# Kernel optimization log

Hardware: AMD Instinct MI355X
Metric: run time of the kernel (lower is better)

## Reference

```python
import jax, jax.numpy as jnp
import numpy as np

H = 8          # num_heads
D = 64         # head_dim
IN = 512       # input_dim
SCALE = D ** -0.5


def setup_inputs() -> dict:
    key = jax.random.key(0)
    ks = jax.random.split(key, 5)
    b, n = 4, 2048
    inner = H * D
    x = jax.random.normal(ks[0], (b, n, IN), dtype=jnp.float32)
    # nn.Linear weights stored as [out, in]; apply as x @ W.T
    Wq = jax.random.normal(ks[1], (inner, IN), dtype=jnp.float32) * (IN ** -0.5)
    Wkv = jax.random.normal(ks[2], (2 * inner, IN), dtype=jnp.float32) * (IN ** -0.5)
    Wo = jax.random.normal(ks[3], (IN, inner), dtype=jnp.float32) * (inner ** -0.5)
    bo = jax.random.normal(ks[4], (IN,), dtype=jnp.float32) * 0.01
    return {"x": x, "Wq": Wq, "Wkv": Wkv, "Wo": Wo, "bo": bo}


def reference(x, Wq, Wkv, Wo, bo):
    b, n, _ = x.shape
    q = jnp.einsum('bni,oi->bno', x, Wq).reshape(b, n, H, D).transpose(0, 2, 1, 3)
    kv = jnp.einsum('bni,oi->bno', x, Wkv)
    k, v = jnp.split(kv, 2, axis=-1)
    k = k.reshape(b, n, H, D).transpose(0, 2, 1, 3)
    v = v.reshape(b, n, H, D).transpose(0, 2, 1, 3)
    attn = jax.nn.softmax(jnp.einsum('bhnd,bhmd->bhnm', q, k) * SCALE, axis=-1)
    # dropout in eval mode: identity
    out = jnp.einsum('bhnm,bhmd->bhnd', attn, v)
    out = out.transpose(0, 2, 1, 3).reshape(b, n, H * D)
    return jnp.einsum('bno,io->bni', out, Wo) + bo
```

## Files before the change

### kernel.cpp

```cpp
#include <hip/hip_runtime.h>
#include <hip/hip_bf16.h>

#define H_ 8
#define D_ 64
#define IN_ 512
#define B_ 4
#define N_ 2048
#define TOK_ (B_*N_)
#define CLOG2_ 0.18033688011112042f

typedef __attribute__((ext_vector_type(8))) short short8;
typedef __attribute__((ext_vector_type(4))) short bs4;
typedef __attribute__((ext_vector_type(4))) float f32x4;

__device__ __forceinline__ unsigned short f2bf(float f) {
  unsigned int u = __float_as_uint(f);
  u += 0x7FFFu + ((u >> 16) & 1u);
  return (unsigned short)(u >> 16);
}

__device__ __forceinline__ short8 cvt8(const float4 a, const float4 b) {
  union { short8 v; __hip_bfloat162 h[4]; } z;
  z.h[0] = __float22bfloat162_rn(make_float2(a.x, a.y));
  z.h[1] = __float22bfloat162_rn(make_float2(a.z, a.w));
  z.h[2] = __float22bfloat162_rn(make_float2(b.x, b.y));
  z.h[3] = __float22bfloat162_rn(make_float2(b.z, b.w));
  return z.v;
}

__device__ __forceinline__ bs4 pack4(float a, float b, float c, float d) {
  union { bs4 v; __hip_bfloat162 h[2]; } z;
  z.h[0] = __float22bfloat162_rn(make_float2(a, b));
  z.h[1] = __float22bfloat162_rn(make_float2(c, d));
  return z.v;
}

__device__ __forceinline__ short8 assemble_p(bs4 pa, bs4 pb) {
  union { bs4 v; unsigned int w[2]; } A, B;
  A.v = pa; B.v = pb;
  auto s0 = __builtin_amdgcn_permlane32_swap(A.w[0], B.w[0], false, false);
  auto s1 = __builtin_amdgcn_permlane32_swap(A.w[1], B.w[1], false, false);
  auto t0 = __builtin_amdgcn_permlane16_swap(s0[0], s0[1], false, false);
  auto t1 = __builtin_amdgcn_permlane16_swap(s1[0], s1[1], false, false);
  union { short8 v; unsigned int w[4]; } R;
  R.w[0] = t0[0];
  R.w[1] = t1[0];
  R.w[2] = t0[1];
  R.w[3] = t1[1];
  return R.v;
}

__device__ __forceinline__ void gld16(const unsigned short* g, unsigned short* l) {
  __builtin_amdgcn_global_load_lds(
      (const __attribute__((address_space(1))) void*)g,
      (__attribute__((address_space(3))) void*)l, 16, 0, 0);
}

__global__ __launch_bounds__(256) void conv_all_kernel(
    const float* __restrict__ x, const float* __restrict__ Wq,
    const float* __restrict__ Wkv, const float* __restrict__ Wo,
    unsigned short* __restrict__ xbf, unsigned short* __restrict__ wbf,
    unsigned short* __restrict__ wobf)
{
  const int b = blockIdx.x;
  const float* src;
  unsigned short* dst;
  size_t base;
  if (b < 2048)      { src = x;   dst = xbf;             base = (size_t)b * 2048; }
  else if (b < 2176) { src = Wq;  dst = wbf;             base = (size_t)(b - 2048) * 2048; }
  else if (b < 2432) { src = Wkv; dst = wbf + 512 * 512; base = (size_t)(b - 2176) * 2048; }
  else               { src = Wo;  dst = wobf;            base = (size_t)(b - 2432) * 2048; }
  size_t i = base + (size_t)threadIdx.x * 8;
  float4 a = *(const float4*)(src + i);
  float4 c = *(const float4*)(src + i + 4);
  *(short8*)(dst + i) = cvt8(a, c);
}

__global__ __launch_bounds__(256) void qkv_gemm_kernel(
    const unsigned short* __restrict__ xbf, const unsigned short* __restrict__ wbf,
    unsigned short* __restrict__ qws, unsigned short* __restrict__ kws,
    unsigned short* __restrict__ vws)
{
  __shared__ __attribute__((aligned(16))) unsigned short sm[128 * 136];

  const int lid = blockIdx.x + (blockIdx.y << 6);
  const int swz = (lid & 7) * 96 + (lid >> 3);
  const int t0 = (swz / 12) * 128;
  const int c0 = (swz % 12) * 128;
  const int cls = c0 >> 9;

  const int tid = threadIdx.x;
  const int wave = tid >> 6, lane = tid & 63;
  const int quad = lane >> 4, l16 = lane & 15;
  const int wm = wave >> 1, wn = wave & 1;

  const int r_ = tid >> 2;
  const int gc = (tid & 3) ^ (r_ & 3);
  const unsigned short* abase = xbf + (size_t)(t0 + r_) * IN_ + gc * 8;
  const unsigned short* bbase = wbf + (size_t)(c0 + r_) * IN_ + gc * 8;

  auto stage = [&](int k0, int buf) {
    unsigned short* sA = sm + buf * 8192;
    unsigned short* sB = sA + 4096;
    gld16(abase + k0,            sA + tid * 8);
    gld16(abase + 64 * IN_ + k0, sA + 2048 + tid * 8);
    gld16(bbase + k0,            sB + tid * 8);
    gld16(bbase + 64 * IN_ + k0, sB + 2048 + tid * 8);
  };

  f32x4 acc[4][4];
  #pragma unroll
  for (int i = 0; i < 4; i++)
    #pragma unroll
    for (int j = 0; j < 4; j++) acc[i][j] = (f32x4){0.f, 0.f, 0.f, 0.f};

  stage(0, 0);

  for (int kt = 0; kt < 16; kt++) {
    const int cur = kt & 1;
    __syncthreads();
    if (kt + 1 < 16) stage((kt + 1) * 32, cur ^ 1);
    const unsigned short* sA = sm + cur * 8192;
    const unsigned short* sB = sA + 4096;
    const int sw = ((quad ^ (l16 & 3)) << 3);
    short8 af[4], bf[4];
    #pragma unroll
    for (int mi = 0; mi < 4; mi++)
      af[mi] = *(const short8*)&sA[(wm * 64 + mi * 16 + l16) * 32 + sw];
    #pragma unroll
    for (int ni = 0; ni < 4; ni++)
      bf[ni] = *(const short8*)&sB[(wn * 64 + ni * 16 + l16) * 32 + sw];
    #pragma unroll
    for (int mi = 0; mi < 4; mi++)
      #pragma unroll
      for (int ni = 0; ni < 4; ni++)
        acc[mi][ni] = __builtin_amdgcn_mfma_f32_16x16x32_bf16(af[mi], bf[ni], acc[mi][ni], 0, 0, 0);
  }

  __syncthreads();

  if (cls < 2) {
    const float qs = (cls == 0) ? CLOG2_ : 1.0f;
    #pragma unroll
    for (int mi = 0; mi < 4; mi++) {
      const int row0 = wm * 64 + mi * 16 + quad * 4;
      #pragma unroll
      for (int ni = 0; ni < 4; ni++) {
        const int col = wn * 64 + ni * 16 + l16;
        #pragma unroll
        for (int r = 0; r < 4; r++)
          sm[(row0 + r) * 136 + col] = f2bf(acc[mi][ni][r] * qs);
      }
    }
    __syncthreads();
    const int row = tid >> 1, half = tid & 1;
    const int t = t0 + row, bb = t >> 11, nn = t & (N_ - 1);
    const int cw = (c0 & 511) + half * 64;
    const int hh = cw >> 6;
    unsigned short* dst = ((cls == 0) ? qws : kws) +
                          ((size_t)(bb * H_ + hh) * N_ + nn) * D_;
    const unsigned short* srcp = &sm[row * 136 + half * 64];
    #pragma unroll
    for (int j = 0; j < 8; j++)
      *(uint4*)(dst + j * 8) = *(const uint4*)(srcp + j * 8);
  } else {
    #pragma unroll
    for (int mi = 0; mi < 4; mi++) {
      const int tk = wm * 64 + mi * 16 + quad * 4;
      #pragma unroll
      for (int ni = 0; ni < 4; ni++) {
        const int col = wn * 64 + ni * 16 + l16;
        bs4 pk4 = pack4(acc[mi][ni][0], acc[mi][ni][1], acc[mi][ni][2], acc[mi][ni][3]);
        *(bs4*)&sm[col * 136 + tk] = pk4;
      }
    }
    __syncthreads();
    const int col = tid >> 1, half = tid & 1;
    const int cw = (c0 - 1024) + col;
    const int hh = cw >> 6, dd = cw & 63;
    const int bb = t0 >> 11, n0 = (t0 & (N_ - 1)) + half * 64;
    unsigned short* dst = vws + ((size_t)(bb * H_ + hh) * D_ + dd) * N_ + n0;
    const unsigned short* srcp = &sm[col * 136 + half * 64];
    #pragma unroll
    for (int j = 0; j < 8; j++)
      *(uint4*)(dst + j * 8) = *(const uint4*)(srcp + j * 8);
  }
}

__global__ __launch_bounds__(256) void attention_kernel(
    const unsigned short* __restrict__ qws,
    const unsigned short* __restrict__ kws,
    const unsigned short* __restrict__ vws,
    unsigned short* __restrict__ ows)
{
  __shared__ __attribute__((aligned(16))) unsigned short sm[2][8192];

  const int lid = blockIdx.x + (blockIdx.y << 5);
  const int swz = ((lid & 7) << 7) + (lid >> 3);
  const int q0 = (swz & 31) * 64;
  const int bh = swz >> 5;
  const int tid = threadIdx.x;
  const int wave = tid >> 6, lane = tid & 63;
  const int quad = lane >> 4, l16 = lane & 15;

  const unsigned short* qbase = qws + (size_t)bh * N_ * D_;
  const unsigned short* kbase = kws + (size_t)bh * N_ * D_;
  const unsigned short* vbase = vws + (size_t)bh * D_ * N_;

  const int qrow = q0 + wave * 16 + l16;
  short8 qf[2];
  #pragma unroll
  for (int kc = 0; kc < 2; kc++)
    qf[kc] = *(const short8*)(qbase + (size_t)qrow * D_ + kc * 32 + quad * 8);

  f32x4 ot[4];
  f32x4 otl;
  #pragma unroll
  for (int db = 0; db < 4; db++) ot[db] = (f32x4){0.f, 0.f, 0.f, 0.f};
  otl = (f32x4){0.f, 0.f, 0.f, 0.f};
  const short8 ones8 = {(short)0x3F80, (short)0x3F80, (short)0x3F80, (short)0x3F80,
                        (short)0x3F80, (short)0x3F80, (short)0x3F80, (short)0x3F80};

  const int r_ = tid >> 3;
  const int gc = (tid & 7) ^ (r_ & 7);
  const unsigned short* kst = kbase + (size_t)r_ * D_ + gc * 8;
  const unsigned short* vst = vbase + (size_t)r_ * N_ + gc * 8;

  {
    unsigned short* Ks = &sm[0][0];
    unsigned short* Vs = &sm[0][4096];
    gld16(kst,                 Ks + tid * 8);
    gld16(kst + 32 * D_,       Ks + 2048 + tid * 8);
    gld16(vst,                 Vs + tid * 8);
    gld16(vst + 32 * N_,       Vs + 2048 + tid * 8);
  }

  for (int kt = 0; kt < N_ / 64; kt++) {
    const int cur = kt & 1;
    __syncthreads();
    if (kt + 1 < N_ / 64) {
      const int k0 = (kt + 1) * 64;
      unsigned short* Ks = &sm[cur ^ 1][0];
      unsigned short* Vs = &sm[cur ^ 1][4096];
      gld16(kst + (size_t)k0 * D_,            Ks + tid * 8);
      gld16(kst + (size_t)(k0 + 32) * D_,     Ks + 2048 + tid * 8);
      gld16(vst + k0,                         Vs + tid * 8);
      gld16(vst + k0 + 32 * N_,               Vs + 2048 + tid * 8);
    }
    const unsigned short* Ks = &sm[cur][0];
    const unsigned short* Vs = &sm[cur][4096];

    f32x4 st[4];
    #pragma unroll
    for (int nb = 0; nb < 4; nb++) st[nb] = (f32x4){0.f, 0.f, 0.f, 0.f};
    #pragma unroll
    for (int kc = 0; kc < 2; kc++) {
      const int sw = (((kc * 4 + quad) ^ (l16 & 7)) << 3);
      #pragma unroll
      for (int nb = 0; nb < 4; nb++) {
        short8 kf = *(const short8*)&Ks[(nb * 16 + l16) * 64 + sw];
        st[nb] = __builtin_amdgcn_mfma_f32_16x16x32_bf16(kf, qf[kc], st[nb], 0, 0, 0);
      }
    }

    bs4 pf[4];
    #pragma unroll
    for (int nb = 0; nb < 4; nb++) {
      float p0 = __builtin_amdgcn_exp2f(st[nb][0]);
      float p1 = __builtin_amdgcn_exp2f(st[nb][1]);
      float p2 = __builtin_amdgcn_exp2f(st[nb][2]);
      float p3 = __builtin_amdgcn_exp2f(st[nb][3]);
      pf[nb] = pack4(p0, p1, p2, p3);
    }

    const short8 pA0 = assemble_p(pf[0], pf[1]);
    const short8 pA1 = assemble_p(pf[2], pf[3]);

    #pragma unroll
    for (int h = 0; h < 2; h++) {
      const short8 pA = h ? pA1 : pA0;
      const int slot = (((h * 4 + quad) ^ (l16 & 7)) << 3);
      #pragma unroll
      for (int db = 0; db < 4; db++) {
        short8 vf8 = *(const short8*)&Vs[(db * 16 + l16) * 64 + slot];
        ot[db] = __builtin_amdgcn_mfma_f32_16x16x32_bf16(vf8, pA, ot[db], 0, 0, 0);
      }
      otl = __builtin_amdgcn_mfma_f32_16x16x32_bf16(ones8, pA, otl, 0, 0, 0);
    }
  }

  const float inv = 1.f / otl[0];
  __syncthreads();
  unsigned short* Os = (unsigned short*)sm;
  #pragma unroll
  for (int db = 0; db < 4; db++) {
    bs4 pk4 = pack4(ot[db][0] * inv, ot[db][1] * inv, ot[db][2] * inv, ot[db][3] * inv);
    *(bs4*)&Os[(wave * 16 + l16) * 72 + db * 16 + quad * 4] = pk4;
  }
  __syncthreads();
  const int b_ = bh >> 3, h_ = bh & 7;
  const int qloc = tid >> 2, chunk = tid & 3;
  unsigned short* dst = ows + ((size_t)b_ * N_ + q0 + qloc) * (H_ * D_) + h_ * 64 + chunk * 16;
  const unsigned short* srcp = &Os[qloc * 72 + chunk * 16];
  *(uint4*)dst = *(const uint4*)srcp;
  *(uint4*)(dst + 8) = *(const uint4*)(srcp + 8);
}

__global__ __launch_bounds__(256) void out_gemm_kernel(
    const unsigned short* __restrict__ ain, const unsigned short* __restrict__ wobf,
    const float* __restrict__ bo, float* __restrict__ y)
{
  __shared__ __attribute__((aligned(16))) unsigned short sm[12288];

  const int lid = blockIdx.x + (blockIdx.y << 6);
  const int swz = ((lid & 7) << 6) + (lid >> 3);
  const int t0 = (swz >> 3) * 128;
  const int c0 = (swz & 7) * 64;
  const int tid = threadIdx.x;
  const int wave = tid >> 6, lane = tid & 63;
  const int quad = lane >> 4, l16 = lane & 15;

  const int r_ = tid >> 2;
  const int gc = (tid & 3) ^ (r_ & 3);
  const unsigned short* abase = ain  + (size_t)(t0 + r_) * IN_ + gc * 8;
  const unsigned short* bbase = wobf + (size_t)(c0 + r_) * IN_ + gc * 8;

  auto stage = [&](int k0, int buf) {
    unsigned short* sA = sm + buf * 6144;
    unsigned short* sB = sA + 4096;
    gld16(abase + k0,            sA + tid * 8);
    gld16(abase + 64 * IN_ + k0, sA + 2048 + tid * 8);
    gld16(bbase + k0,            sB + tid * 8);
  };

  f32x4 acc[2][4];
  #pragma unroll
  for (int i = 0; i < 2; i++)
    #pragma unroll
    for (int j = 0; j < 4; j++) acc[i][j] = (f32x4){0.f, 0.f, 0.f, 0.f};

  stage(0, 0);

  for (int kt = 0; kt < 16; kt++) {
    const int cur = kt & 1;
    __syncthreads();
    if (kt + 1 < 16) stage((kt + 1) * 32, cur ^ 1);
    const unsigned short* sA = sm + cur * 6144;
    const unsigned short* sB = sA + 4096;
    const int sw = ((quad ^ (l16 & 3)) << 3);
    short8 af[2], bf[4];
    #pragma unroll
    for (int mi = 0; mi < 2; mi++)
      af[mi] = *(const short8*)&sA[(wave * 32 + mi * 16 + l16) * 32 + sw];
    #pragma unroll
    for (int ni = 0; ni < 4; ni++)
      bf[ni] = *(const short8*)&sB[(ni * 16 + l16) * 32 + sw];
    #pragma unroll
    for (int mi = 0; mi < 2; mi++)
      #pragma unroll
      for (int ni = 0; ni < 4; ni++)
        acc[mi][ni] = __builtin_amdgcn_mfma_f32_16x16x32_bf16(af[mi], bf[ni], acc[mi][ni], 0, 0, 0);
  }

  #pragma unroll
  for (int mi = 0; mi < 2; mi++) {
    const int t = t0 + wave * 32 + mi * 16 + quad * 4;
    #pragma unroll
    for (int ni = 0; ni < 4; ni++) {
      const int c = c0 + ni * 16 + l16;
      const float bias = bo[c];
      float* dst = y + (size_t)t * IN_ + c;
      dst[0]        = acc[mi][ni][0] + bias;
      dst[IN_]      = acc[mi][ni][1] + bias;
      dst[2 * IN_]  = acc[mi][ni][2] + bias;
      dst[3 * IN_]  = acc[mi][ni][3] + bias;
    }
  }
}

extern "C" void kernel_launch(void* const* d_in, const int* in_sizes, int n_in,
                              void* d_out, int out_size, void* d_ws, size_t ws_size,
                              hipStream_t stream) {
  const float* x   = (const float*)d_in[0];
  const float* Wq  = (const float*)d_in[1];
  const float* Wkv = (const float*)d_in[2];
  const float* Wo  = (const float*)d_in[3];
  const float* bo  = (const float*)d_in[4];
  float* out = (float*)d_out;

  unsigned short* qws  = (unsigned short*)d_ws;
  unsigned short* kws  = qws + (size_t)TOK_ * 512;
  unsigned short* vws  = kws + (size_t)TOK_ * 512;
  unsigned short* ows  = vws + (size_t)TOK_ * 512;
  unsigned short* wbf  = ows + (size_t)TOK_ * 512;
  unsigned short* wobf = wbf + (size_t)1536 * 512;
  unsigned short* xbf  = ows;

  conv_all_kernel<<<dim3(2560), 256, 0, stream>>>(x, Wq, Wkv, Wo, xbf, wbf, wobf);
  qkv_gemm_kernel<<<dim3(TOK_ / 128, 1536 / 128), 256, 0, stream>>>(xbf, wbf, qws, kws, vws);
  attention_kernel<<<dim3(N_ / 64, B_ * H_), 256, 0, stream>>>(qws, kws, vws, ows);
  out_gemm_kernel<<<dim3(TOK_ / 128, 512 / 64), 256, 0, stream>>>(ows, wobf, bo, out);
}
```

Measured before the change: 165.5 us.

## Process two 64-row query blocks per attention workgroup to reuse K/V tiles

Each attention workgroup now handles 128 query rows instead of 64. Each wave keeps two sets of Q fragments and accumulators and reuses every K and V fragment read from shared memory for both row blocks. This halves global K/V streaming and LDS reads per unit of MFMA work, and the launch grid is halved to match. In exchange it uses more registers per thread and gives fewer workgroups to spread across the CUs.

```diff
diff --git a/kernel.cpp b/kernel.cpp
--- a/kernel.cpp
+++ b/kernel.cpp
@@ -195,10 +195,10 @@
 {
   __shared__ __attribute__((aligned(16))) unsigned short sm[2][8192];
 
-  const int lid = blockIdx.x + (blockIdx.y << 5);
-  const int swz = ((lid & 7) << 7) + (lid >> 3);
-  const int q0 = (swz & 31) * 64;
-  const int bh = swz >> 5;
+  const int lid = blockIdx.x + (blockIdx.y << 4);
+  const int swz = ((lid & 7) << 6) + (lid >> 3);
+  const int q0 = (swz & 15) * 128;
+  const int bh = swz >> 4;
   const int tid = threadIdx.x;
   const int wave = tid >> 6, lane = tid & 63;
   const int quad = lane >> 4, l16 = lane & 15;
@@ -207,17 +207,23 @@
   const unsigned short* kbase = kws + (size_t)bh * N_ * D_;
   const unsigned short* vbase = vws + (size_t)bh * D_ * N_;
 
-  const int qrow = q0 + wave * 16 + l16;
-  short8 qf[2];
-  #pragma unroll
-  for (int kc = 0; kc < 2; kc++)
-    qf[kc] = *(const short8*)(qbase + (size_t)qrow * D_ + kc * 32 + quad * 8);
-
-  f32x4 ot[4];
-  f32x4 otl;
-  #pragma unroll
-  for (int db = 0; db < 4; db++) ot[db] = (f32x4){0.f, 0.f, 0.f, 0.f};
-  otl = (f32x4){0.f, 0.f, 0.f, 0.f};
+  short8 qf[2][2];
+  #pragma unroll
+  for (int rb = 0; rb < 2; rb++) {
+    const int qrow = q0 + rb * 64 + wave * 16 + l16;
+    #pragma unroll
+    for (int kc = 0; kc < 2; kc++)
+      qf[rb][kc] = *(const short8*)(qbase + (size_t)qrow * D_ + kc * 32 + quad * 8);
+  }
+
+  f32x4 ot[2][4];
+  f32x4 otl[2];
+  #pragma unroll
+  for (int rb = 0; rb < 2; rb++) {
+    #pragma unroll
+    for (int db = 0; db < 4; db++) ot[rb][db] = (f32x4){0.f, 0.f, 0.f, 0.f};
+    otl[rb] = (f32x4){0.f, 0.f, 0.f, 0.f};
+  }
   const short8 ones8 = {(short)0x3F80, (short)0x3F80, (short)0x3F80, (short)0x3F80,
                         (short)0x3F80, (short)0x3F80, (short)0x3F80, (short)0x3F80};
 
@@ -250,60 +256,77 @@
     const unsigned short* Ks = &sm[cur][0];
     const unsigned short* Vs = &sm[cur][4096];
 
-    f32x4 st[4];
-    #pragma unroll
-    for (int nb = 0; nb < 4; nb++) st[nb] = (f32x4){0.f, 0.f, 0.f, 0.f};
+    f32x4 st[2][4];
+    #pragma unroll
+    for (int rb = 0; rb < 2; rb++)
+      #pragma unroll
+      for (int nb = 0; nb < 4; nb++) st[rb][nb] = (f32x4){0.f, 0.f, 0.f, 0.f};
     #pragma unroll
     for (int kc = 0; kc < 2; kc++) {
       const int sw = (((kc * 4 + quad) ^ (l16 & 7)) << 3);
       #pragma unroll
       for (int nb = 0; nb < 4; nb++) {
         short8 kf = *(const short8*)&Ks[(nb * 16 + l16) * 64 + sw];
-        st[nb] = __builtin_amdgcn_mfma_f32_16x16x32_bf16(kf, qf[kc], st[nb], 0, 0, 0);
+        st[0][nb] = __builtin_amdgcn_mfma_f32_16x16x32_bf16(kf, qf[0][kc], st[0][nb], 0, 0, 0);
+        st[1][nb] = __builtin_amdgcn_mfma_f32_16x16x32_bf16(kf, qf[1][kc], st[1][nb], 0, 0, 0);
       }
     }
 
-    bs4 pf[4];
-    #pragma unroll
-    for (int nb = 0; nb < 4; nb++) {
-      float p0 = __builtin_amdgcn_exp2f(st[nb][0]);
-      float p1 = __builtin_amdgcn_exp2f(st[nb][1]);
-      float p2 = __builtin_amdgcn_exp2f(st[nb][2]);
-      float p3 = __builtin_amdgcn_exp2f(st[nb][3]);
-      pf[nb] = pack4(p0, p1, p2, p3);
-    }
-
-    const short8 pA0 = assemble_p(pf[0], pf[1]);
-    const short8 pA1 = assemble_p(pf[2], pf[3]);
+    short8 pA[2][2];
+    #pragma unroll
+    for (int rb = 0; rb < 2; rb++) {
+      bs4 pf[4];
+      #pragma unroll
+      for (int nb = 0; nb < 4; nb++) {
+        float p0 = __builtin_amdgcn_exp2f(st[rb][nb][0]);
+        float p1 = __builtin_amdgcn_exp2f(st[rb][nb][1]);
+        float p2 = __builtin_amdgcn_exp2f(st[rb][nb][2]);
+        float p3 = __builtin_amdgcn_exp2f(st[rb][nb][3]);
+        pf[nb] = pack4(p0, p1, p2, p3);
+      }
+      pA[rb][0] = assemble_p(pf[0], pf[1]);
+      pA[rb][1] = assemble_p(pf[2], pf[3]);
+    }
 
     #pragma unroll
     for (int h = 0; h < 2; h++) {
-      const short8 pA = h ? pA1 : pA0;
       const int slot = (((h * 4 + quad) ^ (l16 & 7)) << 3);
-      #pragma unroll
-      for (int db = 0; db < 4; db++) {
-        short8 vf8 = *(const short8*)&Vs[(db * 16 + l16) * 64 + slot];
-        ot[db] = __builtin_amdgcn_mfma_f32_16x16x32_bf16(vf8, pA, ot[db], 0, 0, 0);
+      short8 vf8[4];
+      #pragma unroll
+      for (int db = 0; db < 4; db++)
+        vf8[db] = *(const short8*)&Vs[(db * 16 + l16) * 64 + slot];
+      #pragma unroll
+      for (int rb = 0; rb < 2; rb++) {
+        #pragma unroll
+        for (int db = 0; db < 4; db++)
+          ot[rb][db] = __builtin_amdgcn_mfma_f32_16x16x32_bf16(vf8[db], pA[rb][h], ot[rb][db], 0, 0, 0);
+        otl[rb] = __builtin_amdgcn_mfma_f32_16x16x32_bf16(ones8, pA[rb][h], otl[rb], 0, 0, 0);
       }
-      otl = __builtin_amdgcn_mfma_f32_16x16x32_bf16(ones8, pA, otl, 0, 0, 0);
-    }
-  }
-
-  const float inv = 1.f / otl[0];
+    }
+  }
+
+  const float inv0 = 1.f / otl[0][0];
+  const float inv1 = 1.f / otl[1][0];
   __syncthreads();
   unsigned short* Os = (unsigned short*)sm;
   #pragma unroll
-  for (int db = 0; db < 4; db++) {
-    bs4 pk4 = pack4(ot[db][0] * inv, ot[db][1] * inv, ot[db][2] * inv, ot[db][3] * inv);
-    *(bs4*)&Os[(wave * 16 + l16) * 72 + db * 16 + quad * 4] = pk4;
+  for (int rb = 0; rb < 2; rb++) {
+    const float inv = rb ? inv1 : inv0;
+    #pragma unroll
+    for (int db = 0; db < 4; db++) {
+      bs4 pk4 = pack4(ot[rb][db][0] * inv, ot[rb][db][1] * inv,
+                      ot[rb][db][2] * inv, ot[rb][db][3] * inv);
+      *(bs4*)&Os[(rb * 64 + wave * 16 + l16) * 72 + db * 16 + quad * 4] = pk4;
+    }
   }
   __syncthreads();
   const int b_ = bh >> 3, h_ = bh & 7;
-  const int qloc = tid >> 2, chunk = tid & 3;
-  unsigned short* dst = ows + ((size_t)b_ * N_ + q0 + qloc) * (H_ * D_) + h_ * 64 + chunk * 16;
-  const unsigned short* srcp = &Os[qloc * 72 + chunk * 16];
-  *(uint4*)dst = *(const uint4*)srcp;
-  *(uint4*)(dst + 8) = *(const uint4*)(srcp + 8);
+  const int qloc = tid >> 1, chunk = tid & 1;
+  unsigned short* dst = ows + ((size_t)b_ * N_ + q0 + qloc) * (H_ * D_) + h_ * 64 + chunk * 32;
+  const unsigned short* srcp = &Os[qloc * 72 + chunk * 32];
+  #pragma unroll
+  for (int j = 0; j < 4; j++)
+    *(uint4*)(dst + j * 8) = *(const uint4*)(srcp + j * 8);
 }
 
 __global__ __launch_bounds__(256) void out_gemm_kernel(
@@ -398,6 +421,6 @@
 
   conv_all_kernel<<<dim3(2560), 256, 0, stream>>>(x, Wq, Wkv, Wo, xbf, wbf, wobf);
   qkv_gemm_kernel<<<dim3(TOK_ / 128, 1536 / 128), 256, 0, stream>>>(xbf, wbf, qws, kws, vws);
-  attention_kernel<<<dim3(N_ / 64, B_ * H_), 256, 0, stream>>>(qws, kws, vws, ows);
+  attention_kernel<<<dim3(N_ / 128, B_ * H_), 256, 0, stream>>>(qws, kws, vws, ows);
   out_gemm_kernel<<<dim3(TOK_ / 128, 512 / 64), 256, 0, stream>>>(ows, wobf, bo, out);
 }
```

After: 158.3 us. 1.05x faster.
